# Kernel optimization log

Measured on AMD Instinct MI355X. Metric: run time of the kernel, lower is better.

## Reference

```python
import jax, jax.numpy as jnp
import numpy as np

GROUP_SIZE = 64  # quantization group size along in_features (K)


def setup_inputs() -> dict:
    key = jax.random.key(0)
    k1, k2, k3, k4, k5 = jax.random.split(key, 5)
    M, K, N = 32, 8192, 8192
    num_groups = K // GROUP_SIZE
    x = jax.random.normal(k1, (M, K), dtype=jnp.float32)
    # packed int4 weights: two nibbles per byte along K -> [N, K//2]
    packed_weight = jax.random.randint(k2, (N, K // 2), 0, 256, dtype=jnp.int32)
    scales = jax.random.uniform(k3, (N, num_groups), dtype=jnp.float32) * 0.02 + 1e-3
    zeros = jax.random.uniform(k4, (N, num_groups), dtype=jnp.float32) * 15.0
    bias_param = jax.random.normal(k5, (N,), dtype=jnp.float32)
    return {"x": x, "packed_weight": packed_weight, "scales": scales,
            "zeros": zeros, "bias_param": bias_param}


def reference(x, packed_weight, scales, zeros, bias_param):
    # x: [M, K] float; packed_weight: [N, K//2] int (uint8 semantics)
    # scales/zeros: [N, num_groups]; bias_param: [N]
    K = x.shape[-1]
    k = jnp.arange(K)
    shift = (k % 2) * 4                     # low nibble for even k, high for odd
    # unpack int4: q[n, k] in [0, 15]
    q = (packed_weight[:, k // 2] >> shift[None, :]) & 15   # [N, K]
    gidx = k // GROUP_SIZE                                  # [K]
    # group-wise dequant: (q - zero) * scale
    w = (q.astype(jnp.float32) - zeros[:, gidx]) * scales[:, gidx]  # [N, K]
    out = jnp.einsum('mk,nk->mn', x, w) + bias_param[None, :]        # [M, N]
    return out
```

## Files before the change

### kernel.cpp

```cpp
#include <hip/hip_runtime.h>
#include <hip/hip_bf16.h>
#include <stdint.h>


#define KK 8192
#define NN 8192
#define KP 4096
#define NG 128
#define BN 16
#define KSW 64
#define NKS 256
#define KSPLIT 2

typedef __attribute__((ext_vector_type(8))) short short8;
typedef __attribute__((ext_vector_type(4))) float floatx4;
typedef __attribute__((ext_vector_type(4))) int int4v;

__device__ __forceinline__ unsigned pack_bf16x2(float lo, float hi) {
    union { __hip_bfloat162 h; unsigned u; } c;
    c.h = __float22bfloat162_rn(make_float2(lo, hi));
    return c.u;
}

__device__ __forceinline__ unsigned dq2(int q, float sc, float zs) {
    float lo = fmaf((float)(q & 15),        sc, zs);
    float hi = fmaf((float)((q >> 4) & 15), sc, zs);
    unsigned ua = __float_as_uint(lo); ua += 0x7fffu + ((ua >> 16) & 1u);
    unsigned ub = __float_as_uint(hi); ub += 0x7fffu + ((ub >> 16) & 1u);
    return __builtin_amdgcn_perm(ub, ua, 0x07060302);
}

__global__ void prep_kernel(const float* __restrict__ x, const float* __restrict__ bias,
                            ushort* __restrict__ xb, float* __restrict__ out,
                            int xconv_blocks)
{
    const int bx = blockIdx.x;
    if (bx < xconv_blocks) {
        const int tid = bx * 256 + threadIdx.x;
        const int l   = tid & 63;
        const int ks  = (tid >> 6) & 255;
        const int mt  = tid >> 14;
        const int m   = (l & 15) + 16 * mt;
        const int kb  = ks * 32 + (l >> 4) * 8;
        const float* src = x + (size_t)m * KK + kb;
        const float4 a = *(const float4*)(src);
        const float4 b = *(const float4*)(src + 4);
        *(uint4*)(xb + (size_t)tid * 8) =
            make_uint4(pack_bf16x2(a.x, a.y), pack_bf16x2(a.z, a.w),
                       pack_bf16x2(b.x, b.y), pack_bf16x2(b.z, b.w));
    } else {
        const int f4 = (bx - xconv_blocks) * 256 + threadIdx.x;
        const int n4 = f4 & (NN / 4 - 1);
        ((float4*)out)[f4] = ((const float4*)bias)[n4];
    }
}

__global__ __launch_bounds__(256, 2)
void gptq_mfma_main(const int*   __restrict__ pw,
                    const float* __restrict__ scales,
                    const float* __restrict__ zeros,
                    const float* __restrict__ bias,
                    const ushort* __restrict__ xb,
                    float* __restrict__ out)
{
    __shared__ float red[4][2][256];

    const int tid  = threadIdx.x;
    const int lane = tid & 63;
    const int wave = tid >> 6;
    const int n0   = blockIdx.x * BN;
    const int nl   = lane & 15;
    const int kq   = lane >> 4;
    const int ks0  = wave * KSW;

    float scr[32], zsr[32];
    {
        const float* sp = scales + (size_t)(n0 + nl) * NG + wave * 32;
        const float* zp = zeros  + (size_t)(n0 + nl) * NG + wave * 32;
#pragma unroll
        for (int i = 0; i < 8; ++i) {
            const float4 s4 = *(const float4*)(sp + i * 4);
            const float4 z4 = *(const float4*)(zp + i * 4);
            scr[i*4+0] = s4.x; zsr[i*4+0] = -z4.x * s4.x;
            scr[i*4+1] = s4.y; zsr[i*4+1] = -z4.y * s4.y;
            scr[i*4+2] = s4.z; zsr[i*4+2] = -z4.z * s4.z;
            scr[i*4+3] = s4.w; zsr[i*4+3] = -z4.w * s4.w;
        }
    }

    const int* pwp = pw + (size_t)(n0 + nl) * KP + kq * 4;
    const uint4* xfp = (const uint4*)xb;

    floatx4 acc0 = {0.f, 0.f, 0.f, 0.f};
    floatx4 acc1 = {0.f, 0.f, 0.f, 0.f};

    int4v pwb[4];
    uint4 x0b[4], x1b[4];

#pragma unroll
    for (int i = 0; i < 3; ++i) {
        const int ks = ks0 + i;
        pwb[i] = __builtin_nontemporal_load((const int4v*)(pwp + ks * 16));
        x0b[i] = xfp[(size_t)(0 * NKS + ks) * 64 + lane];
        x1b[i] = xfp[(size_t)(1 * NKS + ks) * 64 + lane];
    }

#pragma unroll 4
    for (int i = 0; i < KSW; ++i) {
        const int slot = i & 3;
        if (i + 3 < KSW) {
            const int ks = ks0 + i + 3;
            const int ps = (i + 3) & 3;
            pwb[ps] = __builtin_nontemporal_load((const int4v*)(pwp + ks * 16));
            x0b[ps] = xfp[(size_t)(0 * NKS + ks) * 64 + lane];
            x1b[ps] = xfp[(size_t)(1 * NKS + ks) * 64 + lane];
        }
        const float sc = scr[i >> 1];
        const float zs = zsr[i >> 1];

        union { uint4 v; short8 sv; } bf, a0, a1;
        const int4v p = pwb[slot];
        bf.v.x = dq2(p.x, sc, zs);
        bf.v.y = dq2(p.y, sc, zs);
        bf.v.z = dq2(p.z, sc, zs);
        bf.v.w = dq2(p.w, sc, zs);
        a0.v = x0b[slot];
        a1.v = x1b[slot];
        acc0 = __builtin_amdgcn_mfma_f32_16x16x32_bf16(a0.sv, bf.sv, acc0, 0, 0, 0);
        acc1 = __builtin_amdgcn_mfma_f32_16x16x32_bf16(a1.sv, bf.sv, acc1, 0, 0, 0);
    }

#pragma unroll
    for (int r = 0; r < 4; ++r) {
        const int row = kq * 4 + r;
        red[wave][0][row * 16 + nl] = acc0[r];
        red[wave][1][row * 16 + nl] = acc1[r];
    }
    __syncthreads();

#pragma unroll
    for (int i = 0; i < 2; ++i) {
        const int e   = i * 256 + tid;
        const int mt  = e >> 8;
        const int idx = e & 255;
        const float sv = red[0][mt][idx] + red[1][mt][idx]
                       + red[2][mt][idx] + red[3][mt][idx];
        const int n = n0 + (idx & 15);
        __builtin_nontemporal_store(sv + bias[n],
            out + (size_t)(mt * 16 + (idx >> 4)) * NN + n);
    }
}

__global__ __launch_bounds__(256, 4)
void gptq_mfma_fallback(const int*   __restrict__ pw,
                        const float* __restrict__ scales,
                        const float* __restrict__ zeros,
                        const float* __restrict__ x,
                        float* __restrict__ out)
{
    __shared__ float s_lds[64][BN + 1];
    __shared__ float z_lds[64][BN + 1];
    __shared__ float red[4][2][256];

    const int tid  = threadIdx.x;
    const int lane = tid & 63;
    const int wave = tid >> 6;
    const int kh   = blockIdx.x & (KSPLIT - 1);
    const int n0   = (blockIdx.x >> 1) * BN;
    const int g0   = kh * 64;

    {
        const int r  = tid >> 4;
        const int gb = (tid & 15) * 4;
        const float4 s4 = *(const float4*)(scales + (size_t)(n0 + r) * NG + g0 + gb);
        const float4 z4 = *(const float4*)(zeros  + (size_t)(n0 + r) * NG + g0 + gb);
        s_lds[gb + 0][r] = s4.x; s_lds[gb + 1][r] = s4.y;
        s_lds[gb + 2][r] = s4.z; s_lds[gb + 3][r] = s4.w;
        z_lds[gb + 0][r] = z4.x; z_lds[gb + 1][r] = z4.y;
        z_lds[gb + 2][r] = z4.z; z_lds[gb + 3][r] = z4.w;
    }
    __syncthreads();

    const int nl = lane & 15;
    const int kq = lane >> 4;
    const int* pwp = pw + (size_t)(n0 + nl) * KP + kq * 4;
    const int ks0 = kh * 128 + wave * 32;

    auto load_xfrag = [&](int mt, int ks) -> uint4 {
        const float* src = x + (size_t)(nl + 16 * mt) * KK + ks * 32 + kq * 8;
        const float4 a = *(const float4*)(src);
        const float4 b = *(const float4*)(src + 4);
        return make_uint4(pack_bf16x2(a.x, a.y), pack_bf16x2(a.z, a.w),
                          pack_bf16x2(b.x, b.y), pack_bf16x2(b.z, b.w));
    };

    floatx4 acc0 = {0.f, 0.f, 0.f, 0.f};
    floatx4 acc1 = {0.f, 0.f, 0.f, 0.f};
    int4v pwb[4];
    uint4 x0b[4], x1b[4];

#pragma unroll
    for (int i = 0; i < 3; ++i) {
        const int ks = ks0 + i;
        pwb[i] = __builtin_nontemporal_load((const int4v*)(pwp + ks * 16));
        x0b[i] = load_xfrag(0, ks);
        x1b[i] = load_xfrag(1, ks);
    }

#pragma unroll 4
    for (int i = 0; i < 32; ++i) {
        const int slot = i & 3;
        if (i + 3 < 32) {
            const int ks = ks0 + i + 3;
            const int ps = (i + 3) & 3;
            pwb[ps] = __builtin_nontemporal_load((const int4v*)(pwp + ks * 16));
            x0b[ps] = load_xfrag(0, ks);
            x1b[ps] = load_xfrag(1, ks);
        }
        const int gl  = (wave * 32 + i) >> 1;
        const float sc = s_lds[gl][nl];
        const float zs = -z_lds[gl][nl] * sc;

        union { uint4 v; short8 sv; } bf, a0, a1;
        const int4v p = pwb[slot];
        bf.v.x = dq2(p.x, sc, zs);
        bf.v.y = dq2(p.y, sc, zs);
        bf.v.z = dq2(p.z, sc, zs);
        bf.v.w = dq2(p.w, sc, zs);
        a0.v = x0b[slot];
        a1.v = x1b[slot];
        acc0 = __builtin_amdgcn_mfma_f32_16x16x32_bf16(a0.sv, bf.sv, acc0, 0, 0, 0);
        acc1 = __builtin_amdgcn_mfma_f32_16x16x32_bf16(a1.sv, bf.sv, acc1, 0, 0, 0);
    }

#pragma unroll
    for (int r = 0; r < 4; ++r) {
        const int row = kq * 4 + r;
        red[wave][0][row * 16 + nl] = acc0[r];
        red[wave][1][row * 16 + nl] = acc1[r];
    }
    __syncthreads();

#pragma unroll
    for (int i = 0; i < 2; ++i) {
        const int e   = i * 256 + tid;
        const int mt  = e >> 8;
        const int idx = e & 255;
        const float s = red[0][mt][idx] + red[1][mt][idx] + red[2][mt][idx] + red[3][mt][idx];
        atomicAdd(out + (size_t)(mt * 16 + (idx >> 4)) * NN + n0 + (idx & 15), s);
    }
}

extern "C" void kernel_launch(void* const* d_in, const int* in_sizes, int n_in,
                              void* d_out, int out_size, void* d_ws, size_t ws_size,
                              hipStream_t stream) {
    const float* x      = (const float*)d_in[0];
    const int*   pw     = (const int*)  d_in[1];
    const float* scales = (const float*)d_in[2];
    const float* zeros  = (const float*)d_in[3];
    const float* bias   = (const float*)d_in[4];
    float* out = (float*)d_out;

    const size_t need = (size_t)32768 * 16;
    if (d_ws != nullptr && ws_size >= need) {
        ushort* xb = (ushort*)d_ws;
        prep_kernel<<<128, 256, 0, stream>>>(x, bias, xb, out, 128);
        gptq_mfma_main<<<NN / BN, 256, 0, stream>>>(pw, scales, zeros, bias, xb, out);
    } else {
        prep_kernel<<<256, 256, 0, stream>>>(x, bias, nullptr, out, 0);
        gptq_mfma_fallback<<<512 * KSPLIT, 256, 0, stream>>>(pw, scales, zeros, x, out);
    }
}
```

Measured before the change: 223.7 us.

## Widen main kernel N-tile to 64 with 4-way K split and atomic reduction

The main kernel now covers 64 output columns per block instead of 16, so each x fragment load feeds four dequantized weight fragments. K is split four ways across blocks, and partial sums are combined with atomicAdd into an output that the prep kernel pre-fills with bias. Scales and zero products are staged in LDS rather than held in registers. Weight loads drop the nontemporal hint. The cost is more registers per thread, atomic traffic on the output, and a larger prep launch to write the bias.

```diff
diff --git a/kernel.cpp b/kernel.cpp
--- a/kernel.cpp
+++ b/kernel.cpp
@@ -7,10 +7,10 @@
 #define NN 8192
 #define KP 4096
 #define NG 128
-#define BN 16
-#define KSW 64
+#define BN 64
+#define KSPLIT 4
+#define KSPW 16
 #define NKS 256
-#define KSPLIT 2
 
 typedef __attribute__((ext_vector_type(8))) short short8;
 typedef __attribute__((ext_vector_type(4))) float floatx4;
@@ -59,64 +59,184 @@
 void gptq_mfma_main(const int*   __restrict__ pw,
                     const float* __restrict__ scales,
                     const float* __restrict__ zeros,
-                    const float* __restrict__ bias,
                     const ushort* __restrict__ xb,
                     float* __restrict__ out)
 {
-    __shared__ float red[4][2][256];
+    __shared__ float sc_lds[32][65];
+    __shared__ float zs_lds[32][65];
+    __shared__ float red[4][32][68];
 
     const int tid  = threadIdx.x;
     const int lane = tid & 63;
     const int wave = tid >> 6;
-    const int n0   = blockIdx.x * BN;
+    const int kh   = blockIdx.x & (KSPLIT - 1);
+    const int n0   = (blockIdx.x >> 2) * BN;
     const int nl   = lane & 15;
     const int kq   = lane >> 4;
-    const int ks0  = wave * KSW;
-
-    float scr[32], zsr[32];
+    const int ks0  = kh * 64 + wave * KSPW;
+
     {
-        const float* sp = scales + (size_t)(n0 + nl) * NG + wave * 32;
-        const float* zp = zeros  + (size_t)(n0 + nl) * NG + wave * 32;
-#pragma unroll
-        for (int i = 0; i < 8; ++i) {
-            const float4 s4 = *(const float4*)(sp + i * 4);
-            const float4 z4 = *(const float4*)(zp + i * 4);
-            scr[i*4+0] = s4.x; zsr[i*4+0] = -z4.x * s4.x;
-            scr[i*4+1] = s4.y; zsr[i*4+1] = -z4.y * s4.y;
-            scr[i*4+2] = s4.z; zsr[i*4+2] = -z4.z * s4.z;
-            scr[i*4+3] = s4.w; zsr[i*4+3] = -z4.w * s4.w;
-        }
-    }
-
+        const int r  = tid >> 2;
+        const int go = (tid & 3) * 8;
+        const float* sp = scales + (size_t)(n0 + r) * NG + kh * 32 + go;
+        const float* zp = zeros  + (size_t)(n0 + r) * NG + kh * 32 + go;
+#pragma unroll
+        for (int t = 0; t < 2; ++t) {
+            const float4 s4 = *(const float4*)(sp + t * 4);
+            const float4 z4 = *(const float4*)(zp + t * 4);
+            sc_lds[go + t*4 + 0][r] = s4.x; zs_lds[go + t*4 + 0][r] = -z4.x * s4.x;
+            sc_lds[go + t*4 + 1][r] = s4.y; zs_lds[go + t*4 + 1][r] = -z4.y * s4.y;
+            sc_lds[go + t*4 + 2][r] = s4.z; zs_lds[go + t*4 + 2][r] = -z4.z * s4.z;
+            sc_lds[go + t*4 + 3][r] = s4.w; zs_lds[go + t*4 + 3][r] = -z4.w * s4.w;
+        }
+    }
+    __syncthreads();
+
+    const int* pwp[4];
+#pragma unroll
+    for (int f = 0; f < 4; ++f)
+        pwp[f] = pw + (size_t)(n0 + f * 16 + nl) * KP + kq * 4;
+    const uint4* xfp = (const uint4*)xb;
+
+    floatx4 acc[4][2];
+#pragma unroll
+    for (int f = 0; f < 4; ++f)
+#pragma unroll
+        for (int mt = 0; mt < 2; ++mt)
+            acc[f][mt] = (floatx4){0.f, 0.f, 0.f, 0.f};
+
+    int4v pb[4][4];
+    uint4 xa[4][2];
+
+#pragma unroll
+    for (int i = 0; i < 3; ++i) {
+        const int ks = ks0 + i;
+        xa[i][0] = xfp[(size_t)(0 * NKS + ks) * 64 + lane];
+        xa[i][1] = xfp[(size_t)(1 * NKS + ks) * 64 + lane];
+#pragma unroll
+        for (int f = 0; f < 4; ++f)
+            pb[i][f] = *(const int4v*)(pwp[f] + ks * 16);
+    }
+
+#pragma unroll
+    for (int i = 0; i < KSPW; ++i) {
+        const int slot = i & 3;
+        if (i + 3 < KSPW) {
+            const int ks = ks0 + i + 3;
+            const int ps = (i + 3) & 3;
+            xa[ps][0] = xfp[(size_t)(0 * NKS + ks) * 64 + lane];
+            xa[ps][1] = xfp[(size_t)(1 * NKS + ks) * 64 + lane];
+#pragma unroll
+            for (int f = 0; f < 4; ++f)
+                pb[ps][f] = *(const int4v*)(pwp[f] + ks * 16);
+        }
+        const int gl = (wave * KSPW + i) >> 1;
+
+        union { uint4 v; short8 sv; } a0, a1;
+        a0.v = xa[slot][0];
+        a1.v = xa[slot][1];
+#pragma unroll
+        for (int f = 0; f < 4; ++f) {
+            const float sc = sc_lds[gl][f * 16 + nl];
+            const float zs = zs_lds[gl][f * 16 + nl];
+            union { uint4 v; short8 sv; } bf;
+            const int4v p = pb[slot][f];
+            bf.v.x = dq2(p.x, sc, zs);
+            bf.v.y = dq2(p.y, sc, zs);
+            bf.v.z = dq2(p.z, sc, zs);
+            bf.v.w = dq2(p.w, sc, zs);
+            acc[f][0] = __builtin_amdgcn_mfma_f32_16x16x32_bf16(a0.sv, bf.sv, acc[f][0], 0, 0, 0);
+            acc[f][1] = __builtin_amdgcn_mfma_f32_16x16x32_bf16(a1.sv, bf.sv, acc[f][1], 0, 0, 0);
+        }
+    }
+
+#pragma unroll
+    for (int f = 0; f < 4; ++f)
+#pragma unroll
+        for (int mt = 0; mt < 2; ++mt)
+#pragma unroll
+            for (int r = 0; r < 4; ++r)
+                red[wave][mt * 16 + kq * 4 + r][f * 16 + nl] = acc[f][mt][r];
+    __syncthreads();
+
+#pragma unroll
+    for (int j = 0; j < 8; ++j) {
+        const int e = j * 256 + tid;
+        const int m = e >> 6, c = e & 63;
+        const float s = red[0][m][c] + red[1][m][c] + red[2][m][c] + red[3][m][c];
+        atomicAdd(out + (size_t)m * NN + n0 + c, s);
+    }
+}
+
+__global__ __launch_bounds__(256, 4)
+void gptq_mfma_fallback(const int*   __restrict__ pw,
+                        const float* __restrict__ scales,
+                        const float* __restrict__ zeros,
+                        const float* __restrict__ x,
+                        float* __restrict__ out)
+{
+    __shared__ float s_lds[64][17];
+    __shared__ float z_lds[64][17];
+    __shared__ float red[4][2][256];
+
+    const int tid  = threadIdx.x;
+    const int lane = tid & 63;
+    const int wave = tid >> 6;
+    const int kh   = blockIdx.x & 1;
+    const int n0   = (blockIdx.x >> 1) * 16;
+    const int g0   = kh * 64;
+
+    {
+        const int r  = tid >> 4;
+        const int gb = (tid & 15) * 4;
+        const float4 s4 = *(const float4*)(scales + (size_t)(n0 + r) * NG + g0 + gb);
+        const float4 z4 = *(const float4*)(zeros  + (size_t)(n0 + r) * NG + g0 + gb);
+        s_lds[gb + 0][r] = s4.x; s_lds[gb + 1][r] = s4.y;
+        s_lds[gb + 2][r] = s4.z; s_lds[gb + 3][r] = s4.w;
+        z_lds[gb + 0][r] = z4.x; z_lds[gb + 1][r] = z4.y;
+        z_lds[gb + 2][r] = z4.z; z_lds[gb + 3][r] = z4.w;
+    }
+    __syncthreads();
+
+    const int nl = lane & 15;
+    const int kq = lane >> 4;
     const int* pwp = pw + (size_t)(n0 + nl) * KP + kq * 4;
-    const uint4* xfp = (const uint4*)xb;
+    const int ks0 = kh * 128 + wave * 32;
+
+    auto load_xfrag = [&](int mt, int ks) -> uint4 {
+        const float* src = x + (size_t)(nl + 16 * mt) * KK + ks * 32 + kq * 8;
+        const float4 a = *(const float4*)(src);
+        const float4 b = *(const float4*)(src + 4);
+        return make_uint4(pack_bf16x2(a.x, a.y), pack_bf16x2(a.z, a.w),
+                          pack_bf16x2(b.x, b.y), pack_bf16x2(b.z, b.w));
+    };
 
     floatx4 acc0 = {0.f, 0.f, 0.f, 0.f};
     floatx4 acc1 = {0.f, 0.f, 0.f, 0.f};
-
     int4v pwb[4];
     uint4 x0b[4], x1b[4];
 
 #pragma unroll
     for (int i = 0; i < 3; ++i) {
         const int ks = ks0 + i;
-        pwb[i] = __builtin_nontemporal_load((const int4v*)(pwp + ks * 16));
-        x0b[i] = xfp[(size_t)(0 * NKS + ks) * 64 + lane];
-        x1b[i] = xfp[(size_t)(1 * NKS + ks) * 64 + lane];
+        pwb[i] = *(const int4v*)(pwp + ks * 16);
+        x0b[i] = load_xfrag(0, ks);
+        x1b[i] = load_xfrag(1, ks);
     }
 
 #pragma unroll 4
-    for (int i = 0; i < KSW; ++i) {
+    for (int i = 0; i < 32; ++i) {
         const int slot = i & 3;
-        if (i + 3 < KSW) {
+        if (i + 3 < 32) {
             const int ks = ks0 + i + 3;
             const int ps = (i + 3) & 3;
-            pwb[ps] = __builtin_nontemporal_load((const int4v*)(pwp + ks * 16));
-            x0b[ps] = xfp[(size_t)(0 * NKS + ks) * 64 + lane];
-            x1b[ps] = xfp[(size_t)(1 * NKS + ks) * 64 + lane];
-        }
-        const float sc = scr[i >> 1];
-        const float zs = zsr[i >> 1];
+            pwb[ps] = *(const int4v*)(pwp + ks * 16);
+            x0b[ps] = load_xfrag(0, ks);
+            x1b[ps] = load_xfrag(1, ks);
+        }
+        const int gl  = (wave * 32 + i) >> 1;
+        const float sc = s_lds[gl][nl];
+        const float zs = -z_lds[gl][nl] * sc;
 
         union { uint4 v; short8 sv; } bf, a0, a1;
         const int4v p = pwb[slot];
@@ -143,109 +263,6 @@
         const int e   = i * 256 + tid;
         const int mt  = e >> 8;
         const int idx = e & 255;
-        const float sv = red[0][mt][idx] + red[1][mt][idx]
-                       + red[2][mt][idx] + red[3][mt][idx];
-        const int n = n0 + (idx & 15);
-        __builtin_nontemporal_store(sv + bias[n],
-            out + (size_t)(mt * 16 + (idx >> 4)) * NN + n);
-    }
-}
-
-__global__ __launch_bounds__(256, 4)
-void gptq_mfma_fallback(const int*   __restrict__ pw,
-                        const float* __restrict__ scales,
-                        const float* __restrict__ zeros,
-                        const float* __restrict__ x,
-                        float* __restrict__ out)
-{
-    __shared__ float s_lds[64][BN + 1];
-    __shared__ float z_lds[64][BN + 1];
-    __shared__ float red[4][2][256];
-
-    const int tid  = threadIdx.x;
-    const int lane = tid & 63;
-    const int wave = tid >> 6;
-    const int kh   = blockIdx.x & (KSPLIT - 1);
-    const int n0   = (blockIdx.x >> 1) * BN;
-    const int g0   = kh * 64;
-
-    {
-        const int r  = tid >> 4;
-        const int gb = (tid & 15) * 4;
-        const float4 s4 = *(const float4*)(scales + (size_t)(n0 + r) * NG + g0 + gb);
-        const float4 z4 = *(const float4*)(zeros  + (size_t)(n0 + r) * NG + g0 + gb);
-        s_lds[gb + 0][r] = s4.x; s_lds[gb + 1][r] = s4.y;
-        s_lds[gb + 2][r] = s4.z; s_lds[gb + 3][r] = s4.w;
-        z_lds[gb + 0][r] = z4.x; z_lds[gb + 1][r] = z4.y;
-        z_lds[gb + 2][r] = z4.z; z_lds[gb + 3][r] = z4.w;
-    }
-    __syncthreads();
-
-    const int nl = lane & 15;
-    const int kq = lane >> 4;
-    const int* pwp = pw + (size_t)(n0 + nl) * KP + kq * 4;
-    const int ks0 = kh * 128 + wave * 32;
-
-    auto load_xfrag = [&](int mt, int ks) -> uint4 {
-        const float* src = x + (size_t)(nl + 16 * mt) * KK + ks * 32 + kq * 8;
-        const float4 a = *(const float4*)(src);
-        const float4 b = *(const float4*)(src + 4);
-        return make_uint4(pack_bf16x2(a.x, a.y), pack_bf16x2(a.z, a.w),
-                          pack_bf16x2(b.x, b.y), pack_bf16x2(b.z, b.w));
-    };
-
-    floatx4 acc0 = {0.f, 0.f, 0.f, 0.f};
-    floatx4 acc1 = {0.f, 0.f, 0.f, 0.f};
-    int4v pwb[4];
-    uint4 x0b[4], x1b[4];
-
-#pragma unroll
-    for (int i = 0; i < 3; ++i) {
-        const int ks = ks0 + i;
-        pwb[i] = __builtin_nontemporal_load((const int4v*)(pwp + ks * 16));
-        x0b[i] = load_xfrag(0, ks);
-        x1b[i] = load_xfrag(1, ks);
-    }
-
-#pragma unroll 4
-    for (int i = 0; i < 32; ++i) {
-        const int slot = i & 3;
-        if (i + 3 < 32) {
-            const int ks = ks0 + i + 3;
-            const int ps = (i + 3) & 3;
-            pwb[ps] = __builtin_nontemporal_load((const int4v*)(pwp + ks * 16));
-            x0b[ps] = load_xfrag(0, ks);
-            x1b[ps] = load_xfrag(1, ks);
-        }
-        const int gl  = (wave * 32 + i) >> 1;
-        const float sc = s_lds[gl][nl];
-        const float zs = -z_lds[gl][nl] * sc;
-
-        union { uint4 v; short8 sv; } bf, a0, a1;
-        const int4v p = pwb[slot];
-        bf.v.x = dq2(p.x, sc, zs);
-        bf.v.y = dq2(p.y, sc, zs);
-        bf.v.z = dq2(p.z, sc, zs);
-        bf.v.w = dq2(p.w, sc, zs);
-        a0.v = x0b[slot];
-        a1.v = x1b[slot];
-        acc0 = __builtin_amdgcn_mfma_f32_16x16x32_bf16(a0.sv, bf.sv, acc0, 0, 0, 0);
-        acc1 = __builtin_amdgcn_mfma_f32_16x16x32_bf16(a1.sv, bf.sv, acc1, 0, 0, 0);
-    }
-
-#pragma unroll
-    for (int r = 0; r < 4; ++r) {
-        const int row = kq * 4 + r;
-        red[wave][0][row * 16 + nl] = acc0[r];
-        red[wave][1][row * 16 + nl] = acc1[r];
-    }
-    __syncthreads();
-
-#pragma unroll
-    for (int i = 0; i < 2; ++i) {
-        const int e   = i * 256 + tid;
-        const int mt  = e >> 8;
-        const int idx = e & 255;
         const float s = red[0][mt][idx] + red[1][mt][idx] + red[2][mt][idx] + red[3][mt][idx];
         atomicAdd(out + (size_t)(mt * 16 + (idx >> 4)) * NN + n0 + (idx & 15), s);
     }
@@ -264,10 +281,10 @@
     const size_t need = (size_t)32768 * 16;
     if (d_ws != nullptr && ws_size >= need) {
         ushort* xb = (ushort*)d_ws;
-        prep_kernel<<<128, 256, 0, stream>>>(x, bias, xb, out, 128);
-        gptq_mfma_main<<<NN / BN, 256, 0, stream>>>(pw, scales, zeros, bias, xb, out);
+        prep_kernel<<<128 + 256, 256, 0, stream>>>(x, bias, xb, out, 128);
+        gptq_mfma_main<<<(NN / BN) * KSPLIT, 256, 0, stream>>>(pw, scales, zeros, xb, out);
     } else {
         prep_kernel<<<256, 256, 0, stream>>>(x, bias, nullptr, out, 0);
-        gptq_mfma_fallback<<<512 * KSPLIT, 256, 0, stream>>>(pw, scales, zeros, x, out);
-    }
-}
+        gptq_mfma_fallback<<<1024, 256, 0, stream>>>(pw, scales, zeros, x, out);
+    }
+}
```

New measurement: 208.9 us. -6.6%, faster.
